# Kernel optimization log

Measured on AMD Instinct MI355X. Metric: run time of the kernel, lower is better.

## Reference

```python
import jax, jax.numpy as jnp
import numpy as np

B, T, W = 4, 2048, 1024
K, G = 7, 8            # kernel_size, groups
Cg = W // G            # channels per group
SE_R = 16              # SE reduction ratio
LN_EPS = 1e-5


def setup_inputs() -> dict:
    key = jax.random.key(0)
    ks = jax.random.split(key, 8)
    h = jax.random.normal(ks[0], (B, T, W), jnp.float32)
    # mask: True = padding; valid prefix of random length per row
    lengths = jax.random.randint(ks[1], (B,), T // 2, T + 1)
    mask = jnp.arange(T)[None, :] >= lengths[:, None]
    s_w = np.float32(1.0 / np.sqrt(W))
    return dict(
        h=h,
        mask=mask,
        offset_w=jax.random.normal(ks[2], (W, K), jnp.float32) * 0.01,
        offset_b=jnp.zeros((K,), jnp.float32),
        conv_w=jax.random.normal(ks[3], (G, Cg, Cg, K), jnp.float32) * np.float32(1.0 / np.sqrt(Cg * K)),
        conv_b=jnp.zeros((W,), jnp.float32),
        ln_g=jnp.ones((W,), jnp.float32),
        ln_b=jnp.zeros((W,), jnp.float32),
        se_w1=jax.random.normal(ks[4], (W, W // SE_R), jnp.float32) * s_w,
        se_b1=jnp.zeros((W // SE_R,), jnp.float32),
        se_w2=jax.random.normal(ks[5], (W // SE_R, W), jnp.float32) * np.float32(1.0 / np.sqrt(W // SE_R)),
        se_b2=jnp.zeros((W,), jnp.float32),
        proj_w=jax.random.normal(ks[6], (W, 1), jnp.float32) * s_w,
        proj_b=jnp.zeros((1,), jnp.float32),
    )


def deform_conv1d(h, offset_w, offset_b, conv_w, conv_b):
    # h: [B,T,W]. Learned per-(position, tap) fractional offsets; linear interp gather;
    # grouped conv combine. conv_w: [G, out_per_group, in_per_group, K].
    Bn, Tn, Wn = h.shape
    pad = (K - 1) // 2
    offsets = h @ offset_w + offset_b                                   # [B,T,K]
    base = (jnp.arange(Tn, dtype=jnp.float32)[None, :, None]
            + (jnp.arange(K, dtype=jnp.float32) - pad)[None, None, :])  # [1,T,K]
    pos = jnp.clip(base + offsets, 0.0, Tn - 1.0)                       # [B,T,K]
    p0 = jnp.floor(pos).astype(jnp.int32)
    p1 = jnp.minimum(p0 + 1, Tn - 1)
    frac = (pos - p0.astype(jnp.float32))[..., None]                    # [B,T,K,1]
    gather = jax.vmap(lambda hb, ib: hb[ib])                            # [T,W],[T,K] -> [T,K,W]
    sampled = gather(h, p0) * (1.0 - frac) + gather(h, p1) * frac       # [B,T,K,W]
    sg = sampled.reshape(Bn, Tn, K, G, Cg)
    out = jnp.einsum('btkgc,gock->btgo', sg, conv_w).reshape(Bn, Tn, Wn)
    return out + conv_b


def layer_norm(x, g, b):
    mu = jnp.mean(x, axis=-1, keepdims=True)
    var = jnp.mean(jnp.square(x - mu), axis=-1, keepdims=True)
    return (x - mu) * jax.lax.rsqrt(var + LN_EPS) * g + b


def se_block(x, mask, w1, b1, w2, b2):
    valid = (~mask).astype(x.dtype)[..., None]                          # [B,T,1]
    lengths = jnp.clip(jnp.sum(valid, axis=1), 1.0)                     # [B,1]
    s = jnp.sum(x * valid, axis=1) / lengths                            # [B,W]
    gate = jax.nn.sigmoid(jax.nn.relu(s @ w1 + b1) @ w2 + b2)           # [B,W]
    return x * gate[:, None, :]


def reference(h, mask, offset_w, offset_b, conv_w, conv_b, ln_g, ln_b,
              se_w1, se_b1, se_w2, se_b2, proj_w, proj_b):
    x = layer_norm(deform_conv1d(h, offset_w, offset_b, conv_w, conv_b), ln_g, ln_b)
    x = se_block(x, mask, se_w1, se_b1, se_w2, se_b2)
    # dropout: identity in eval mode (p handled outside reference)
    valid = (~mask).astype(x.dtype)[..., None]
    x = x * valid                                                       # masked_fill(mask, 0)
    lengths = jnp.clip(jnp.sum(valid, axis=1), 1.0)                     # [B,1]
    pooled = jnp.sum(x, axis=1) / lengths                               # [B,W]
    return jnp.squeeze(pooled @ proj_w + proj_b, axis=-1)               # [B]
```

## Files before the change

### kernel.cpp

```cpp
#include <hip/hip_runtime.h>
#include <hip/hip_bf16.h>

#define Bdim 4
#define Tdim 2048
#define Wdim 1024
#define Kdim 7
#define Gdim 8
#define Cg   128
#define Hdim 64
#define TT   64

typedef __attribute__((ext_vector_type(8))) short short8v;
typedef __attribute__((ext_vector_type(4))) float float4v;

__device__ __forceinline__ short f2bf(float x) {
    union { float f; unsigned u; } v; v.f = x;
    unsigned r = v.u + 0x7fff + ((v.u >> 16) & 1);
    return (short)(r >> 16);
}

__device__ __forceinline__ unsigned pack2bf(float lo, float hi) {
    return __builtin_amdgcn_perm(__float_as_uint(hi) + 0x8000u,
                                 __float_as_uint(lo) + 0x8000u, 0x07060302u);
}

__device__ __forceinline__ short8v lerp_pack(uint4 a, uint4 b, float f) {
    union { uint4 u; short8v s; } r;
    const unsigned* pa = (const unsigned*)&a;
    const unsigned* pb = (const unsigned*)&b;
    unsigned* pr = (unsigned*)&r.u;
#pragma unroll
    for (int d = 0; d < 4; d++) {
        float alo = __uint_as_float(pa[d] << 16);
        float ahi = __uint_as_float(pa[d] & 0xffff0000u);
        float blo = __uint_as_float(pb[d] << 16);
        float bhi = __uint_as_float(pb[d] & 0xffff0000u);
        float rlo = alo + f * (blo - alo);
        float rhi = ahi + f * (bhi - ahi);
        pr[d] = pack2bf(rlo, rhi);
    }
    return r.s;
}

__global__ __launch_bounds__(256) void k_pre(const float* __restrict__ conv_w,
                                             short* __restrict__ Wtb,
                                             const float* __restrict__ h,
                                             const float* __restrict__ offset_w,
                                             const float* __restrict__ offset_b,
                                             float* __restrict__ pos,
                                             ushort* __restrict__ h16,
                                             float* __restrict__ s_sum,
                                             float* __restrict__ rowstat) {
    int tid = threadIdx.x;
    if (blockIdx.x < 448) {
        if (blockIdx.x == 0) {
#pragma unroll
            for (int i = 0; i < 16; i++) s_sum[tid + i * 256] = 0.f;
        }
        if (blockIdx.x < 64) rowstat[blockIdx.x * 256 + tid] = 0.f;
        int i = blockIdx.x * 256 + tid;
        int cb = i & 15;
        int o = (i >> 4) & 127;
        int gk = i >> 11;
        int k = gk % Kdim, g = gk / Kdim;
        const float* src = conv_w + ((size_t)(g * Cg + o) * Cg + cb * 8) * Kdim + k;
        short8v pk;
#pragma unroll
        for (int j = 0; j < 8; j++) pk[j] = f2bf(src[(size_t)j * Kdim]);
        short8v* Wtb8 = (short8v*)Wtb;
        Wtb8[(size_t)gk * 2048 + o * 16 + cb] = pk;
        return;
    }
    int lane = tid & 63, wv = tid >> 6;
    int bt = (blockIdx.x - 448) * 4 + wv;
    int t = bt & (Tdim - 1);
    const float* row = h + (size_t)bt * Wdim;
    float acc[Kdim];
#pragma unroll
    for (int k = 0; k < Kdim; k++) acc[k] = 0.f;
#pragma unroll
    for (int j = 0; j < 4; j++) {
        int c = lane * 4 + j * 256;
        float4 hv = *(const float4*)(row + c);
        const float* ow = offset_w + (size_t)c * Kdim;
#pragma unroll
        for (int k = 0; k < Kdim; k++)
            acc[k] += hv.x * ow[k] + hv.y * ow[Kdim + k] + hv.z * ow[2 * Kdim + k]
                    + hv.w * ow[3 * Kdim + k];
        ushort4 hp;
        hp.x = (ushort)f2bf(hv.x); hp.y = (ushort)f2bf(hv.y);
        hp.z = (ushort)f2bf(hv.z); hp.w = (ushort)f2bf(hv.w);
        *(ushort4*)(h16 + (size_t)bt * Wdim + c) = hp;
    }
#pragma unroll
    for (int k = 0; k < Kdim; k++) {
#pragma unroll
        for (int m = 32; m > 0; m >>= 1) acc[k] += __shfl_xor(acc[k], m);
    }
    if (lane < Kdim) {
        float o = acc[lane] + offset_b[lane];
        float base = (float)t + (float)(lane - 3);
        float p = fminf(fmaxf(base + o, 0.f), (float)(Tdim - 1));
        pos[bt * Kdim + lane] = p;
    }
}

__global__ __launch_bounds__(256, 4) void k_conv(const ushort* __restrict__ h16,
                                                 const short* __restrict__ Wtb,
                                                 const float* __restrict__ conv_b,
                                                 const float* __restrict__ pos,
                                                 ushort* __restrict__ y16,
                                                 float* __restrict__ rowstat) {
    __shared__ short8v sA8[2][TT * 16];
    __shared__ float posl[TT * 8];

    int blk = blockIdx.x;
    int g  = blk & 7;
    int tc = (blk >> 3) & 31;
    int b  = blk >> 8;
    int t0 = tc * TT;
    int tid = threadIdx.x;
    int lane = tid & 63, wv = tid >> 6;
    int r15 = lane & 15, q = lane >> 4;

    const ushort* hb = h16 + (size_t)(b * Tdim) * Wdim + g * Cg;
    const short8v* WtbV = (const short8v*)Wtb + (size_t)(g * Kdim) * 2048;

    int scb = tid & 15;
    int sr0 = tid >> 4;

    {
        int base = (b * Tdim + t0) * Kdim;
        for (int u = tid; u < TT * Kdim; u += 256) {
            int r = u / 7, kk = u - r * 7;
            posl[r * 8 + kk] = pos[base + u];
        }
    }
    __syncthreads();

    float4v acc[4][2];
#pragma unroll
    for (int tt = 0; tt < 4; tt++)
#pragma unroll
        for (int n = 0; n < 2; n++) acc[tt][n] = (float4v){0.f, 0.f, 0.f, 0.f};

    float fr[4];
    uint4 glo[4], ghi[4];
#pragma unroll
    for (int i = 0; i < 4; i++) {
        int r = sr0 + i * 16;
        float p = posl[r * 8 + 0];
        int p0 = (int)p;
        fr[i] = p - (float)p0;
        int p1 = min(p0 + 1, Tdim - 1);
        glo[i] = *(const uint4*)(hb + (size_t)p0 * Wdim + scb * 8);
        ghi[i] = *(const uint4*)(hb + (size_t)p1 * Wdim + scb * 8);
    }

#pragma unroll 1
    for (int k = 0; k < Kdim; k++) {
        short8v bfr[8];
#pragma unroll
        for (int n = 0; n < 2; n++)
#pragma unroll
            for (int kk = 0; kk < 4; kk++)
                bfr[n * 4 + kk] =
                    WtbV[(size_t)k * 2048 + (wv * 32 + n * 16 + r15) * 16 + kk * 4 + q];
        short8v* buf = sA8[k & 1];
#pragma unroll
        for (int i = 0; i < 4; i++) {
            int r = sr0 + i * 16;
            buf[r * 16 + (scb ^ (r & 7))] = lerp_pack(glo[i], ghi[i], fr[i]);
        }
        __syncthreads();
        if (k < Kdim - 1) {
#pragma unroll
            for (int i = 0; i < 4; i++) {
                int r = sr0 + i * 16;
                float p = posl[r * 8 + k + 1];
                int p0 = (int)p;
                fr[i] = p - (float)p0;
                int p1 = min(p0 + 1, Tdim - 1);
                glo[i] = *(const uint4*)(hb + (size_t)p0 * Wdim + scb * 8);
                ghi[i] = *(const uint4*)(hb + (size_t)p1 * Wdim + scb * 8);
            }
        }
#pragma unroll
        for (int tt = 0; tt < 4; tt++) {
            int r = tt * 16 + r15;
            short8v af[4];
#pragma unroll
            for (int kk = 0; kk < 4; kk++)
                af[kk] = buf[r * 16 + ((kk * 4 + q) ^ (r & 7))];
#pragma unroll
            for (int kk = 0; kk < 4; kk++) {
#pragma unroll
                for (int n = 0; n < 2; n++)
                    acc[tt][n] = __builtin_amdgcn_mfma_f32_16x16x32_bf16(
                        af[kk], bfr[n * 4 + kk], acc[tt][n], 0, 0, 0);
            }
        }
    }
    __syncthreads();
    float* ep = (float*)sA8;
#pragma unroll
    for (int n = 0; n < 2; n++) {
        int colb = wv * 32 + n * 16 + r15;
        float bias = conv_b[g * Cg + colb];
#pragma unroll
        for (int tt = 0; tt < 4; tt++)
#pragma unroll
            for (int j = 0; j < 4; j++) {
                int row = tt * 16 + q * 4 + j;
                ep[row * 128 + (colb ^ ((row & 7) << 2))] = acc[tt][n][j] + bias;
            }
    }
    __syncthreads();
    int row = tid >> 2, c0 = (tid & 3) * 32;
    int sw = (row & 7) << 2;
    ushort* yp = y16 + (size_t)(b * Tdim + t0 + row) * Wdim + g * Cg + c0;
    float s_part = 0.f, q_part = 0.f;
#pragma unroll
    for (int s = 0; s < 4; s++) {
        float4 va = *(const float4*)&ep[row * 128 + ((c0 + s * 8) ^ sw)];
        float4 vb = *(const float4*)&ep[row * 128 + ((c0 + s * 8 + 4) ^ sw)];
        s_part += va.x + va.y + va.z + va.w + vb.x + vb.y + vb.z + vb.w;
        q_part += va.x * va.x + va.y * va.y + va.z * va.z + va.w * va.w
                + vb.x * vb.x + vb.y * vb.y + vb.z * vb.z + vb.w * vb.w;
        uint4 o;
        o.x = pack2bf(va.x, va.y);
        o.y = pack2bf(va.z, va.w);
        o.z = pack2bf(vb.x, vb.y);
        o.w = pack2bf(vb.z, vb.w);
        *(uint4*)(yp + s * 8) = o;
    }
    s_part += __shfl_xor(s_part, 1); s_part += __shfl_xor(s_part, 2);
    q_part += __shfl_xor(q_part, 1); q_part += __shfl_xor(q_part, 2);
    if ((tid & 3) == 0) {
        atomicAdd(&rowstat[(b * Tdim + t0 + row) * 2 + 0], s_part);
        atomicAdd(&rowstat[(b * Tdim + t0 + row) * 2 + 1], q_part);
    }
}

__global__ __launch_bounds__(256) void k_lnpool(const ushort* __restrict__ y16,
                                                const int* __restrict__ mask,
                                                const float* __restrict__ rowstat,
                                                float* __restrict__ s_sum) {
    int blk = blockIdx.x;
    int b = blk >> 6, ch = blk & 63;
    int tid = threadIdx.x;
    int c0 = tid * 4;
    float a0 = 0.f, a1 = 0.f, a2 = 0.f, a3 = 0.f;
    for (int i = 0; i < 32; i++) {
        int t = ch * 32 + i;
        if (mask[b * Tdim + t]) continue;
        float st = rowstat[(b * Tdim + t) * 2 + 0];
        float sq = rowstat[(b * Tdim + t) * 2 + 1];
        float mu = st * (1.f / Wdim);
        float inv = rsqrtf(sq * (1.f / Wdim) - mu * mu + 1e-5f);
        uint2 u = *(const uint2*)(y16 + (size_t)(b * Tdim + t) * Wdim + c0);
        float v0 = __uint_as_float(u.x << 16);
        float v1 = __uint_as_float(u.x & 0xffff0000u);
        float v2 = __uint_as_float(u.y << 16);
        float v3 = __uint_as_float(u.y & 0xffff0000u);
        a0 += (v0 - mu) * inv; a1 += (v1 - mu) * inv;
        a2 += (v2 - mu) * inv; a3 += (v3 - mu) * inv;
    }
    atomicAdd(&s_sum[b * Wdim + c0 + 0], a0);
    atomicAdd(&s_sum[b * Wdim + c0 + 1], a1);
    atomicAdd(&s_sum[b * Wdim + c0 + 2], a2);
    atomicAdd(&s_sum[b * Wdim + c0 + 3], a3);
}

__global__ __launch_bounds__(256) void k_sefinal(const float* __restrict__ s_sum,
                                                 const int* __restrict__ mask,
                                                 const float* __restrict__ ln_g,
                                                 const float* __restrict__ ln_b,
                                                 const float* __restrict__ w1,
                                                 const float* __restrict__ b1,
                                                 const float* __restrict__ w2,
                                                 const float* __restrict__ b2,
                                                 const float* __restrict__ projw,
                                                 const float* __restrict__ projb,
                                                 float* __restrict__ out) {
    int b = blockIdx.x, tid = threadIdx.x;
    __shared__ float s[Wdim];
    __shared__ float hred[4][Hdim];
    __shared__ float hid[Hdim];
    __shared__ float rbuf[4];
    __shared__ float sLinv;
    int lane = tid & 63, wv = tid >> 6;

    int cnt = 0;
    for (int t = tid; t < Tdim; t += 256) cnt += (mask[b * Tdim + t] ? 0 : 1);
    float fc = (float)cnt;
#pragma unroll
    for (int off = 32; off > 0; off >>= 1) fc += __shfl_down(fc, off);
    if (lane == 0) rbuf[wv] = fc;
    __syncthreads();
    if (tid == 0) {
        float L = rbuf[0] + rbuf[1] + rbuf[2] + rbuf[3];
        sLinv = 1.f / fmaxf(L, 1.f);
    }
    __syncthreads();
    float Linv = sLinv;

    int w4 = tid * 4;
    float4 a = *(const float4*)(s_sum + b * Wdim + w4);
    float4 gg = *(const float4*)(ln_g + w4);
    float4 bb = *(const float4*)(ln_b + w4);
    s[w4 + 0] = gg.x * (a.x * Linv) + bb.x;
    s[w4 + 1] = gg.y * (a.y * Linv) + bb.y;
    s[w4 + 2] = gg.z * (a.z * Linv) + bb.z;
    s[w4 + 3] = gg.w * (a.w * Linv) + bb.w;
    __syncthreads();

    int j = tid & 63, p = tid >> 6;
    float ha = 0.f;
    for (int w = p * 256; w < (p + 1) * 256; ++w) ha += s[w] * w1[(size_t)w * Hdim + j];
    hred[p][j] = ha;
    __syncthreads();
    if (tid < Hdim)
        hid[tid] = fmaxf(hred[0][tid] + hred[1][tid] + hred[2][tid] + hred[3][tid] + b1[tid], 0.f);
    __syncthreads();

    float part = 0.f;
    for (int w = tid; w < Wdim; w += 256) {
        float ga = b2[w];
#pragma unroll 8
        for (int j2 = 0; j2 < Hdim; j2++) ga += hid[j2] * w2[(size_t)j2 * Wdim + w];
        float gate = 1.f / (1.f + expf(-ga));
        part += s[w] * gate * projw[w];
    }
#pragma unroll
    for (int off = 32; off > 0; off >>= 1) part += __shfl_down(part, off);
    __syncthreads();
    if (lane == 0) rbuf[wv] = part;
    __syncthreads();
    if (tid == 0) out[b] = rbuf[0] + rbuf[1] + rbuf[2] + rbuf[3] + projb[0];
}

extern "C" void kernel_launch(void* const* d_in, const int* in_sizes, int n_in,
                              void* d_out, int out_size, void* d_ws, size_t ws_size,
                              hipStream_t stream) {
    const float* h        = (const float*)d_in[0];
    const int*   mask     = (const int*)d_in[1];
    const float* offset_w = (const float*)d_in[2];
    const float* offset_b = (const float*)d_in[3];
    const float* conv_w   = (const float*)d_in[4];
    const float* conv_b   = (const float*)d_in[5];
    const float* ln_g     = (const float*)d_in[6];
    const float* ln_b     = (const float*)d_in[7];
    const float* se_w1    = (const float*)d_in[8];
    const float* se_b1    = (const float*)d_in[9];
    const float* se_w2    = (const float*)d_in[10];
    const float* se_b2    = (const float*)d_in[11];
    const float* proj_w   = (const float*)d_in[12];
    const float* proj_b   = (const float*)d_in[13];
    float* out = (float*)d_out;

    char* wsb = (char*)d_ws;
    float*  pos     = (float*)(wsb);
    ushort* h16     = (ushort*)(wsb + 229376);
    short*  Wtb     = (short*)(wsb + 17006592);
    ushort* y16     = (ushort*)(wsb + 18841600);
    float*  s_sum   = (float*)(wsb + 35618816);
    float*  rowstat = (float*)(wsb + 35635200);

    k_pre<<<dim3(448 + Bdim * Tdim / 4), dim3(256), 0, stream>>>(conv_w, Wtb, h, offset_w,
                                                                 offset_b, pos, h16, s_sum,
                                                                 rowstat);
    k_conv<<<dim3(Bdim * (Tdim / TT) * Gdim), dim3(256), 0, stream>>>(h16, Wtb, conv_b,
                                                                      pos, y16, rowstat);
    k_lnpool<<<dim3(Bdim * 64), dim3(256), 0, stream>>>(y16, mask, rowstat, s_sum);
    k_sefinal<<<dim3(Bdim), dim3(256), 0, stream>>>(s_sum, mask, ln_g, ln_b,
                                                    se_w1, se_b1, se_w2, se_b2,
                                                    proj_w, proj_b, out);
}
```

Measured before the change: 106.6 us.

## Prefetch conv weights across taps, replace atomics with partial sums, relax launch bounds

```diff
diff --git a/kernel.cpp b/kernel.cpp
--- a/kernel.cpp
+++ b/kernel.cpp
@@ -49,14 +49,9 @@
                                              const float* __restrict__ offset_b,
                                              float* __restrict__ pos,
                                              ushort* __restrict__ h16,
-                                             float* __restrict__ s_sum,
                                              float* __restrict__ rowstat) {
     int tid = threadIdx.x;
     if (blockIdx.x < 448) {
-        if (blockIdx.x == 0) {
-#pragma unroll
-            for (int i = 0; i < 16; i++) s_sum[tid + i * 256] = 0.f;
-        }
         if (blockIdx.x < 64) rowstat[blockIdx.x * 256 + tid] = 0.f;
         int i = blockIdx.x * 256 + tid;
         int cb = i & 15;
@@ -105,7 +100,7 @@
     }
 }
 
-__global__ __launch_bounds__(256, 4) void k_conv(const ushort* __restrict__ h16,
+__global__ __launch_bounds__(256, 3) void k_conv(const ushort* __restrict__ h16,
                                                  const short* __restrict__ Wtb,
                                                  const float* __restrict__ conv_b,
                                                  const float* __restrict__ pos,
@@ -146,6 +141,7 @@
 
     float fr[4];
     uint4 glo[4], ghi[4];
+    short8v bfr[8];
 #pragma unroll
     for (int i = 0; i < 4; i++) {
         int r = sr0 + i * 16;
@@ -156,16 +152,14 @@
         glo[i] = *(const uint4*)(hb + (size_t)p0 * Wdim + scb * 8);
         ghi[i] = *(const uint4*)(hb + (size_t)p1 * Wdim + scb * 8);
     }
+#pragma unroll
+    for (int n = 0; n < 2; n++)
+#pragma unroll
+        for (int kk = 0; kk < 4; kk++)
+            bfr[n * 4 + kk] = WtbV[(wv * 32 + n * 16 + r15) * 16 + kk * 4 + q];
 
 #pragma unroll 1
     for (int k = 0; k < Kdim; k++) {
-        short8v bfr[8];
-#pragma unroll
-        for (int n = 0; n < 2; n++)
-#pragma unroll
-            for (int kk = 0; kk < 4; kk++)
-                bfr[n * 4 + kk] =
-                    WtbV[(size_t)k * 2048 + (wv * 32 + n * 16 + r15) * 16 + kk * 4 + q];
         short8v* buf = sA8[k & 1];
 #pragma unroll
         for (int i = 0; i < 4; i++) {
@@ -185,6 +179,7 @@
                 ghi[i] = *(const uint4*)(hb + (size_t)p1 * Wdim + scb * 8);
             }
         }
+        __builtin_amdgcn_sched_barrier(0);
 #pragma unroll
         for (int tt = 0; tt < 4; tt++) {
             int r = tt * 16 + r15;
@@ -199,6 +194,15 @@
                     acc[tt][n] = __builtin_amdgcn_mfma_f32_16x16x32_bf16(
                         af[kk], bfr[n * 4 + kk], acc[tt][n], 0, 0, 0);
             }
+        }
+        __builtin_amdgcn_sched_barrier(0);
+        if (k < Kdim - 1) {
+#pragma unroll
+            for (int n = 0; n < 2; n++)
+#pragma unroll
+                for (int kk = 0; kk < 4; kk++)
+                    bfr[n * 4 + kk] =
+                        WtbV[(size_t)(k + 1) * 2048 + (wv * 32 + n * 16 + r15) * 16 + kk * 4 + q];
         }
     }
     __syncthreads();
@@ -245,7 +249,7 @@
 __global__ __launch_bounds__(256) void k_lnpool(const ushort* __restrict__ y16,
                                                 const int* __restrict__ mask,
                                                 const float* __restrict__ rowstat,
-                                                float* __restrict__ s_sum) {
+                                                float* __restrict__ part) {
     int blk = blockIdx.x;
     int b = blk >> 6, ch = blk & 63;
     int tid = threadIdx.x;
@@ -254,10 +258,9 @@
     for (int i = 0; i < 32; i++) {
         int t = ch * 32 + i;
         if (mask[b * Tdim + t]) continue;
-        float st = rowstat[(b * Tdim + t) * 2 + 0];
-        float sq = rowstat[(b * Tdim + t) * 2 + 1];
-        float mu = st * (1.f / Wdim);
-        float inv = rsqrtf(sq * (1.f / Wdim) - mu * mu + 1e-5f);
+        float2 st = *(const float2*)(rowstat + (b * Tdim + t) * 2);
+        float mu = st.x * (1.f / Wdim);
+        float inv = rsqrtf(st.y * (1.f / Wdim) - mu * mu + 1e-5f);
         uint2 u = *(const uint2*)(y16 + (size_t)(b * Tdim + t) * Wdim + c0);
         float v0 = __uint_as_float(u.x << 16);
         float v1 = __uint_as_float(u.x & 0xffff0000u);
@@ -266,13 +269,10 @@
         a0 += (v0 - mu) * inv; a1 += (v1 - mu) * inv;
         a2 += (v2 - mu) * inv; a3 += (v3 - mu) * inv;
     }
-    atomicAdd(&s_sum[b * Wdim + c0 + 0], a0);
-    atomicAdd(&s_sum[b * Wdim + c0 + 1], a1);
-    atomicAdd(&s_sum[b * Wdim + c0 + 2], a2);
-    atomicAdd(&s_sum[b * Wdim + c0 + 3], a3);
-}
-
-__global__ __launch_bounds__(256) void k_sefinal(const float* __restrict__ s_sum,
+    *(float4*)(part + (size_t)blk * Wdim + c0) = (float4){a0, a1, a2, a3};
+}
+
+__global__ __launch_bounds__(256) void k_sefinal(const float* __restrict__ part,
                                                  const int* __restrict__ mask,
                                                  const float* __restrict__ ln_g,
                                                  const float* __restrict__ ln_b,
@@ -306,7 +306,11 @@
     float Linv = sLinv;
 
     int w4 = tid * 4;
-    float4 a = *(const float4*)(s_sum + b * Wdim + w4);
+    float4 a = {0.f, 0.f, 0.f, 0.f};
+    for (int chh = 0; chh < 64; chh++) {
+        float4 p = *(const float4*)(part + (size_t)(b * 64 + chh) * Wdim + w4);
+        a.x += p.x; a.y += p.y; a.z += p.z; a.w += p.w;
+    }
     float4 gg = *(const float4*)(ln_g + w4);
     float4 bb = *(const float4*)(ln_b + w4);
     s[w4 + 0] = gg.x * (a.x * Linv) + bb.x;
@@ -324,18 +328,18 @@
         hid[tid] = fmaxf(hred[0][tid] + hred[1][tid] + hred[2][tid] + hred[3][tid] + b1[tid], 0.f);
     __syncthreads();
 
-    float part = 0.f;
+    float part2 = 0.f;
     for (int w = tid; w < Wdim; w += 256) {
         float ga = b2[w];
 #pragma unroll 8
         for (int j2 = 0; j2 < Hdim; j2++) ga += hid[j2] * w2[(size_t)j2 * Wdim + w];
         float gate = 1.f / (1.f + expf(-ga));
-        part += s[w] * gate * projw[w];
-    }
-#pragma unroll
-    for (int off = 32; off > 0; off >>= 1) part += __shfl_down(part, off);
-    __syncthreads();
-    if (lane == 0) rbuf[wv] = part;
+        part2 += s[w] * gate * projw[w];
+    }
+#pragma unroll
+    for (int off = 32; off > 0; off >>= 1) part2 += __shfl_down(part2, off);
+    __syncthreads();
+    if (lane == 0) rbuf[wv] = part2;
     __syncthreads();
     if (tid == 0) out[b] = rbuf[0] + rbuf[1] + rbuf[2] + rbuf[3] + projb[0];
 }
@@ -364,16 +368,15 @@
     ushort* h16     = (ushort*)(wsb + 229376);
     short*  Wtb     = (short*)(wsb + 17006592);
     ushort* y16     = (ushort*)(wsb + 18841600);
-    float*  s_sum   = (float*)(wsb + 35618816);
-    float*  rowstat = (float*)(wsb + 35635200);
+    float*  rowstat = (float*)(wsb + 35618816);
+    float*  part    = (float*)(wsb + 35684352);
 
     k_pre<<<dim3(448 + Bdim * Tdim / 4), dim3(256), 0, stream>>>(conv_w, Wtb, h, offset_w,
-                                                                 offset_b, pos, h16, s_sum,
-                                                                 rowstat);
+                                                                 offset_b, pos, h16, rowstat);
     k_conv<<<dim3(Bdim * (Tdim / TT) * Gdim), dim3(256), 0, stream>>>(h16, Wtb, conv_b,
                                                                       pos, y16, rowstat);
-    k_lnpool<<<dim3(Bdim * 64), dim3(256), 0, stream>>>(y16, mask, rowstat, s_sum);
-    k_sefinal<<<dim3(Bdim), dim3(256), 0, stream>>>(s_sum, mask, ln_g, ln_b,
+    k_lnpool<<<dim3(Bdim * 64), dim3(256), 0, stream>>>(y16, mask, rowstat, part);
+    k_sefinal<<<dim3(Bdim), dim3(256), 0, stream>>>(part, mask, ln_g, ln_b,
                                                     se_w1, se_b1, se_w2, se_b2,
                                                     proj_w, proj_b, out);
 }
```

Measured after the change: 105.8 us. No clear change (-0.7%).
